# Performance work log

Hardware: AMD Instinct MI355X
Metric: run time of the kernel (lower is better)

## Reference

```python
import jax, jax.numpy as jnp
import numpy as np
import math

B, T, D = 2, 2048, 1024
H = 16
HD = D // H
DFF = 4096
EPS = 1e-5


def setup_inputs() -> dict:
    key = jax.random.key(0)
    ks = jax.random.split(key, 11)
    s = 0.02
    return {
        "x": jax.random.normal(ks[0], (B, T, D), dtype=jnp.float32),
        "scale1": jnp.ones((D,), jnp.float32),
        "scale2": jnp.ones((D,), jnp.float32),
        "Wqkv": jax.random.normal(ks[1], (D, 3 * D), jnp.float32) * s,
        "bqkv": jnp.zeros((3 * D,), jnp.float32),
        "Wo": jax.random.normal(ks[2], (D, D), jnp.float32) * s,
        "bo": jnp.zeros((D,), jnp.float32),
        "W1": jax.random.normal(ks[3], (D, DFF), jnp.float32) * s,
        "b1": jnp.zeros((DFF,), jnp.float32),
        "W2": jax.random.normal(ks[4], (DFF, D), jnp.float32) * s,
        "b2": jnp.zeros((D,), jnp.float32),
    }


def rmsnorm(x, scale):
    # Faithful to source: norm = ||x||/sqrt(d); out = scale * x / (norm + eps)
    d = x.shape[-1]
    norm = jnp.linalg.norm(x, axis=-1, keepdims=True) * (1.0 / math.sqrt(d))
    return scale * x / (norm + EPS)


def attention(x, Wqkv, bqkv, Wo, bo):
    b, t, c = x.shape
    qkv = x @ Wqkv + bqkv                       # [B,T,3D]
    qkv = qkv.reshape(b, t, 3, H, HD)
    q, k, v = qkv[:, :, 0], qkv[:, :, 1], qkv[:, :, 2]   # [B,T,H,HD]
    scores = jnp.einsum("bqhd,bkhd->bhqk", q, k) / math.sqrt(HD)
    w = jax.nn.softmax(scores, axis=-1)
    out = jnp.einsum("bhqk,bkhd->bqhd", w, v).reshape(b, t, c)
    return out @ Wo + bo


def reference(x, scale1, scale2, Wqkv, bqkv, Wo, bo, W1, b1, W2, b2):
    x = x + attention(rmsnorm(x, scale1), Wqkv, bqkv, Wo, bo)
    h = rmsnorm(x, scale2)
    ff = (jax.nn.gelu(h @ W1 + b1, approximate=False)) @ W2 + b2
    return x + ff
```

## Files before the change

kernel.cpp:

```cpp
#include <hip/hip_runtime.h>
#include <hip/hip_bf16.h>
#include <math.h>

typedef unsigned short u16;
typedef __bf16 bf16x8 __attribute__((ext_vector_type(8)));
typedef float f32x4 __attribute__((ext_vector_type(4)));
typedef unsigned int u32x2 __attribute__((ext_vector_type(2)));

#define B_   2
#define T_   2048
#define D_   1024
#define H_   16
#define HD_  64
#define DFF_ 4096
#define M_TOK (B_*T_)

__device__ __forceinline__ u16 f2bf(float f){
  unsigned u = __float_as_uint(f);
  u += 0x7fff + ((u>>16)&1);
  return (u16)(u>>16);
}

__device__ __forceinline__ void gl2lds16(const void* g, void* l){
  __builtin_amdgcn_global_load_lds((const __attribute__((address_space(1))) void*)g,
                                   (__attribute__((address_space(3))) void*)l, 16, 0, 0);
}

__device__ __forceinline__ unsigned lds_u32(const void* p){
  return (unsigned)(uintptr_t)(const __attribute__((address_space(3))) void*)p;
}

__device__ __forceinline__ u32x2 tr_read(unsigned addr){
  u32x2 d;
  asm volatile("ds_read_b64_tr_b16 %0, %1" : "=v"(d) : "v"(addr));
  return d;
}
__device__ __forceinline__ u32x2 tr_read512(unsigned addr){
  u32x2 d;
  asm volatile("ds_read_b64_tr_b16 %0, %1 offset:512" : "=v"(d) : "v"(addr));
  return d;
}
__device__ __forceinline__ bf16x8 pack8(u32x2 a, u32x2 b){
  union { u32x2 u[2]; bf16x8 v; } x; x.u[0]=a; x.u[1]=b; return x.v;
}
__device__ __forceinline__ unsigned cvt_pk_bf16(float a, float b){
  unsigned r;
  asm("v_cvt_pk_bf16_f32 %0, %1, %2" : "=v"(r) : "v"(a), "v"(b));
  return r;
}

__device__ __forceinline__ void block_barrier(){
  asm volatile("" ::: "memory");
  __builtin_amdgcn_s_barrier();
  __builtin_amdgcn_sched_barrier(0);
  asm volatile("" ::: "memory");
}

__device__ __forceinline__ int xcd_chunk(int orig, int nwg){
  int q = nwg >> 3, r = nwg & 7;
  int x = orig & 7, s = orig >> 3;
  return (x < r ? x*(q+1) : r*(q+1) + (x-r)*q) + s;
}

__global__ __launch_bounds__(256) void k_transpose_bf16(const float* __restrict__ in,
                                                        u16* __restrict__ out, int K, int N){
  __shared__ float t[32][33];
  int bx = blockIdx.x*32, by = blockIdx.y*32;
  int tx = threadIdx.x, ty = threadIdx.y;
  #pragma unroll
  for(int i=ty;i<32;i+=8) t[i][tx] = in[(size_t)(by+i)*N + bx + tx];
  __syncthreads();
  #pragma unroll
  for(int i=ty;i<32;i+=8) out[(size_t)(bx+i)*K + by + tx] = f2bf(t[tx][i]);
}

__global__ __launch_bounds__(256) void k_rmsnorm_bf16(const float* __restrict__ x,
                                                      const float* __restrict__ scale,
                                                      u16* __restrict__ out){
  int row = blockIdx.x;
  int tid = threadIdx.x;
  int lane = tid&63, wave = tid>>6;
  const float4* xr = (const float4*)(x + (size_t)row*D_);
  float4 v = xr[tid];
  float ss = v.x*v.x + v.y*v.y + v.z*v.z + v.w*v.w;
  #pragma unroll
  for(int o=1;o<64;o<<=1) ss += __shfl_xor(ss, o);
  __shared__ float red[4];
  if(lane==0) red[wave]=ss;
  __syncthreads();
  float tot = red[0]+red[1]+red[2]+red[3];
  float inv = 1.0f/(sqrtf(tot*(1.0f/D_)) + 1e-5f);
  const float4* sr = (const float4*)scale;
  float4 s4 = sr[tid];
  u16* o4 = out + (size_t)row*D_ + tid*4;
  o4[0]=f2bf(v.x*s4.x*inv); o4[1]=f2bf(v.y*s4.y*inv);
  o4[2]=f2bf(v.z*s4.z*inv); o4[3]=f2bf(v.w*s4.w*inv);
}

template<int EPI>
__global__ __launch_bounds__(512,2) void k_gemm256(const u16* __restrict__ A, const u16* __restrict__ Bt,
                                                   const float* __restrict__ bias,
                                                   void* __restrict__ Cout, int M, int N, int K, int nbx){
  __shared__ u16 LDS[4][16384];
  const int tid = threadIdx.x;
  const int lane = tid&63, wave = tid>>6;
  const int lo = lane&15, hi = lane>>4;
  const int wm = wave>>2, wn = wave&3;
  const int l = xcd_chunk(blockIdx.x, gridDim.x);
  const int row0 = (l % nbx)*256, col0 = (l / nbx)*256;
  f32x4 acc[8][4];
  #pragma unroll
  for(int m=0;m<8;m++)
    #pragma unroll
    for(int n=0;n<4;n++) acc[m][n] = (f32x4){0.f,0.f,0.f,0.f};
  const u16* Ag = A + (size_t)row0*K;
  const u16* Bg = Bt + (size_t)col0*K;
  const int NT = K>>5;

  const int cc0 = tid, cc1 = tid+512;
  const size_t s0 = (size_t)(cc0>>2)*K + (size_t)((((cc0&3)^((cc0>>3)&3)))<<3);
  const size_t s1 = (size_t)(cc1>>2)*K + (size_t)((((cc1&3)^((cc1>>3)&3)))<<3);

  #define STAGE_A(t) { const u16* Ab = Ag + (size_t)(t)*32; char* d = (char*)LDS[(t)&3]; \
    gl2lds16(Ab + s0, d + cc0*16); gl2lds16(Ab + s1, d + cc1*16); }
  #define STAGE_B(t) { const u16* Bb = Bg + (size_t)(t)*32; char* d = (char*)LDS[(t)&3] + 16384; \
    gl2lds16(Bb + s0, d + cc0*16); gl2lds16(Bb + s1, d + cc1*16); }

  STAGE_A(0); STAGE_B(0); STAGE_A(1); STAGE_B(1); STAGE_A(2); STAGE_B(2);

  const unsigned slot = (unsigned)((hi ^ ((lo>>1)&3))<<4);
  for(int t=0;t<NT;t++){
    if(t<NT-2)       { asm volatile("s_waitcnt vmcnt(8)" ::: "memory"); }
    else if(t==NT-2) { asm volatile("s_waitcnt vmcnt(4)" ::: "memory"); }
    else             { asm volatile("s_waitcnt vmcnt(0)" ::: "memory"); }
    block_barrier();
    const char* bufp = (const char*)LDS[t&3];
    const char* ap = bufp + (wm*128 + lo)*64 + slot;
    const char* bp = bufp + 16384 + (wn*64 + lo)*64 + slot;

    if(t+3<NT) STAGE_A(t+3);
    __builtin_amdgcn_sched_barrier(0);
    bf16x8 a0[4], b[4];
    #pragma unroll
    for(int m=0;m<4;m++) a0[m] = *(const bf16x8*)(ap + m*1024);
    #pragma unroll
    for(int n=0;n<4;n++) b[n]  = *(const bf16x8*)(bp + n*1024);
    __builtin_amdgcn_s_setprio(1);
    #pragma unroll
    for(int m=0;m<4;m++)
      #pragma unroll
      for(int n=0;n<4;n++)
        acc[m][n] = __builtin_amdgcn_mfma_f32_16x16x32_bf16(a0[m], b[n], acc[m][n], 0,0,0);
    __builtin_amdgcn_s_setprio(0);

    if(t+3<NT) STAGE_B(t+3);
    __builtin_amdgcn_sched_barrier(0);
    bf16x8 a1[4];
    #pragma unroll
    for(int m=0;m<4;m++) a1[m] = *(const bf16x8*)(ap + 4096 + m*1024);
    __builtin_amdgcn_s_setprio(1);
    #pragma unroll
    for(int m=0;m<4;m++)
      #pragma unroll
      for(int n=0;n<4;n++)
        acc[m+4][n] = __builtin_amdgcn_mfma_f32_16x16x32_bf16(a1[m], b[n], acc[m+4][n], 0,0,0);
    __builtin_amdgcn_s_setprio(0);
  }
  #undef STAGE_A
  #undef STAGE_B

  #pragma unroll
  for(int m=0;m<8;m++){
    #pragma unroll
    for(int n=0;n<4;n++){
      #pragma unroll
      for(int r=0;r<4;r++){
        int row = row0 + wm*128 + m*16 + hi*4 + r;
        int col = col0 + wn*64 + n*16 + lo;
        float v = acc[m][n][r] + bias[col];
        if constexpr(EPI==2){
          v = 0.5f*v*(1.0f + erff(v*0.70710678118f));
        }
        ((u16*)Cout)[(size_t)row*N + col] = f2bf(v);
      }
    }
  }
}

template<int EPI>
__global__ __launch_bounds__(256) void k_gemm(const u16* __restrict__ A, const u16* __restrict__ Bt,
                                              const float* __restrict__ bias, const float* __restrict__ res,
                                              void* __restrict__ Cout, int M, int N, int K, int nbx){
  __shared__ u16 As[128*32];
  __shared__ u16 Bs[128*32];
  int tid = threadIdx.x;
  int lane = tid&63, wave = tid>>6;
  int lo = lane&15, hi = lane>>4;
  int wr = wave>>1, wc = wave&1;
  const int l = xcd_chunk(blockIdx.x, gridDim.x);
  int row0 = (l % nbx)*128, col0 = (l / nbx)*128;
  f32x4 acc[4][4];
  #pragma unroll
  for(int m=0;m<4;m++)
    #pragma unroll
    for(int n=0;n<4;n++) acc[m][n] = (f32x4){0.f,0.f,0.f,0.f};
  const u16* Ag = A + (size_t)row0*K;
  const u16* Bg = Bt + (size_t)col0*K;
  const unsigned sw = (unsigned)((hi^((lo>>1)&3))*16);
  for(int k0=0;k0<K;k0+=32){
    __syncthreads();
    #pragma unroll
    for(int c=tid;c<512;c+=256){
      gl2lds16(Ag + (size_t)(c>>2)*K + k0 + (size_t)(((c&3)^((c>>3)&3))<<3), (char*)As + c*16);
      gl2lds16(Bg + (size_t)(c>>2)*K + k0 + (size_t)(((c&3)^((c>>3)&3))<<3), (char*)Bs + c*16);
    }
    __syncthreads();
    const char* ab = (const char*)As + (wr*64+lo)*64;
    const char* bb = (const char*)Bs + (wc*64+lo)*64;
    bf16x8 a[4], b[4];
    #pragma unroll
    for(int m=0;m<4;m++) a[m] = *(const bf16x8*)(ab + m*1024 + sw);
    #pragma unroll
    for(int n=0;n<4;n++) b[n] = *(const bf16x8*)(bb + n*1024 + sw);
    #pragma unroll
    for(int m=0;m<4;m++)
      #pragma unroll
      for(int n=0;n<4;n++)
        acc[m][n] = __builtin_amdgcn_mfma_f32_16x16x32_bf16(a[m], b[n], acc[m][n], 0,0,0);
  }
  #pragma unroll
  for(int m=0;m<4;m++){
    #pragma unroll
    for(int n=0;n<4;n++){
      #pragma unroll
      for(int r=0;r<4;r++){
        int row = row0 + wr*64 + m*16 + hi*4 + r;
        int col = col0 + wc*64 + n*16 + lo;
        float v = acc[m][n][r] + bias[col];
        if constexpr(EPI==1){
          ((float*)Cout)[(size_t)row*N + col] = v + res[(size_t)row*N + col];
        } else if constexpr(EPI==2){
          v = 0.5f*v*(1.0f + erff(v*0.70710678118f));
          ((u16*)Cout)[(size_t)row*N + col] = f2bf(v);
        } else {
          ((u16*)Cout)[(size_t)row*N + col] = f2bf(v);
        }
      }
    }
  }
}

__global__ __launch_bounds__(256) void k_gemm_pk(const u16* __restrict__ A, const u16* __restrict__ Bt,
                                                 float* __restrict__ P, int M, int N, int K){
  __shared__ u16 As[128*32];
  __shared__ u16 Bs[128*32];
  int tid = threadIdx.x;
  int lane = tid&63, wave = tid>>6;
  int lo = lane&15, hi = lane>>4;
  int wr = wave>>1, wc = wave&1;
  const int l = xcd_chunk(blockIdx.x, gridDim.x);
  const int nbx = M>>7, nby = N>>7;
  int row0 = (l % nbx)*128;
  int col0 = ((l / nbx) % nby)*128;
  int kc   = l / (nbx*nby);
  int klen = K/2, kbeg = kc*klen;
  f32x4 acc[4][4];
  #pragma unroll
  for(int m=0;m<4;m++)
    #pragma unroll
    for(int n=0;n<4;n++) acc[m][n] = (f32x4){0.f,0.f,0.f,0.f};
  const u16* Ag = A + (size_t)row0*K + kbeg;
  const u16* Bg = Bt + (size_t)col0*K + kbeg;
  const unsigned sw = (unsigned)((hi^((lo>>1)&3))*16);
  for(int k0=0;k0<klen;k0+=32){
    __syncthreads();
    #pragma unroll
    for(int c=tid;c<512;c+=256){
      gl2lds16(Ag + (size_t)(c>>2)*K + k0 + (size_t)(((c&3)^((c>>3)&3))<<3), (char*)As + c*16);
      gl2lds16(Bg + (size_t)(c>>2)*K + k0 + (size_t)(((c&3)^((c>>3)&3))<<3), (char*)Bs + c*16);
    }
    __syncthreads();
    const char* ab = (const char*)As + (wr*64+lo)*64;
    const char* bb = (const char*)Bs + (wc*64+lo)*64;
    bf16x8 a[4], b[4];
    #pragma unroll
    for(int m=0;m<4;m++) a[m] = *(const bf16x8*)(ab + m*1024 + sw);
    #pragma unroll
    for(int n=0;n<4;n++) b[n] = *(const bf16x8*)(bb + n*1024 + sw);
    #pragma unroll
    for(int m=0;m<4;m++)
      #pragma unroll
      for(int n=0;n<4;n++)
        acc[m][n] = __builtin_amdgcn_mfma_f32_16x16x32_bf16(a[m], b[n], acc[m][n], 0,0,0);
  }
  float* Pk = P + (size_t)kc*M*N;
  #pragma unroll
  for(int m=0;m<4;m++)
    #pragma unroll
    for(int n=0;n<4;n++)
      #pragma unroll
      for(int r=0;r<4;r++){
        int row = row0 + wr*64 + m*16 + hi*4 + r;
        int col = col0 + wc*64 + n*16 + lo;
        Pk[(size_t)row*N + col] = acc[m][n][r];
      }
}

__global__ __launch_bounds__(256) void k_ff2_reduce(const float* __restrict__ P,
                                                    const float* __restrict__ bias,
                                                    const float* __restrict__ res,
                                                    float* __restrict__ out){
  const size_t total4 = (size_t)M_TOK*D_/4;
  const float4* p0 = (const float4*)P;
  const float4* p1 = (const float4*)(P + (size_t)M_TOK*D_);
  const float4* rr = (const float4*)res;
  const float4* bb = (const float4*)bias;
  float4* oo = (float4*)out;
  for(size_t i = (size_t)blockIdx.x*256 + threadIdx.x; i < total4; i += (size_t)gridDim.x*256){
    float4 a = p0[i], b = p1[i], r = rr[i], c = bb[i & (D_/4 - 1)];
    float4 o;
    o.x = (a.x+b.x)+(c.x+r.x);
    o.y = (a.y+b.y)+(c.y+r.y);
    o.z = (a.z+b.z)+(c.z+r.z);
    o.w = (a.w+b.w)+(c.w+r.w);
    oo[i] = o;
  }
}

__global__ __launch_bounds__(256,4) void k_attn(const u16* __restrict__ qkv, u16* __restrict__ O){
  __shared__ alignas(16) u16 Ks[2][4096];
  __shared__ alignas(16) u16 Vs[2][4096];
  __shared__ alignas(16) u16 Ps[4][1024];
  const int l = xcd_chunk(blockIdx.x, 1024);
  const int qt = l & 31, bh = l >> 5;
  const int h = bh & 15, b = bh >> 4;
  const int tid = threadIdx.x, lane = tid&63, wave = tid>>6;
  const int lo = lane&15, hi = lane>>4, l7 = lane&7;
  const u16* qkvB = qkv + (size_t)b*T_*3072;
  const int hoff = h*64;
  const float C2 = 0.18033688f;

  const int q0 = qt*64 + wave*16;
  const u16* qp = qkvB + (size_t)(q0+lo)*3072 + hoff + hi*8;
  bf16x8 aq0 = *(const bf16x8*)qp;
  bf16x8 aq1 = *(const bf16x8*)(qp+32);

  size_t sK[2], sV[2];
  {
    int cc[2] = {tid, tid+256};
    #pragma unroll
    for(int i=0;i<2;i++){
      int c = cc[i];
      sK[i] = (size_t)(c>>3)*3072 + 1024 + hoff + (((c&7)^((c>>3)&7))<<3);
      int kv = ((c>>5)<<2) + ((c>>1)&3);
      int d0 = (((c&31)>>3)<<4) | ((c&1)<<3);
      sV[i] = (size_t)kv*3072 + 2048 + hoff + d0;
    }
  }
  const unsigned kb0 = (unsigned)lo*128 + (unsigned)((hi^l7))*16;
  const unsigned kb1 = (unsigned)lo*128 + (unsigned)(((hi|4)^l7))*16;
  const unsigned vtr = (unsigned)hi*1024 + (unsigned)lo*2;
  const unsigned swzQ = (unsigned)(lo&7)<<4;

  f32x4 oac[4];
  #pragma unroll
  for(int n=0;n<4;n++) oac[n] = (f32x4){0.f,0.f,0.f,0.f};
  float mrow = -1e30f;
  float lsum = 0.f;

  {
    char* kd = (char*)Ks[0]; char* vd = (char*)Vs[0];
    gl2lds16(qkvB + sK[0], kd + tid*16);
    gl2lds16(qkvB + sK[1], kd + tid*16 + 4096);
    gl2lds16(qkvB + sV[0], vd + tid*16);
    gl2lds16(qkvB + sV[1], vd + tid*16 + 4096);
  }
  int buf = 0;
  for(int t=0;t<T_/64;t++){
    __syncthreads();
    if(t < T_/64-1){
      size_t koff = (size_t)(t+1)*64*3072;
      char* kd = (char*)Ks[buf^1]; char* vd = (char*)Vs[buf^1];
      gl2lds16(qkvB + koff + sK[0], kd + tid*16);
      gl2lds16(qkvB + koff + sK[1], kd + tid*16 + 4096);
      gl2lds16(qkvB + koff + sV[0], vd + tid*16);
      gl2lds16(qkvB + koff + sV[1], vd + tid*16 + 4096);
    }
    const char* K_ = (const char*)Ks[buf];
    u16* P_ = Ps[wave];

    f32x4 s[4];
    __builtin_amdgcn_s_setprio(1);
    #pragma unroll
    for(int n=0;n<4;n++){
      bf16x8 k0f = *(const bf16x8*)(K_ + n*2048 + kb0);
      bf16x8 k1f = *(const bf16x8*)(K_ + n*2048 + kb1);
      f32x4 z = (f32x4){0.f,0.f,0.f,0.f};
      z = __builtin_amdgcn_mfma_f32_16x16x32_bf16(k0f, aq0, z, 0,0,0);
      z = __builtin_amdgcn_mfma_f32_16x16x32_bf16(k1f, aq1, z, 0,0,0);
      s[n] = z;
    }
    __builtin_amdgcn_s_setprio(0);

    float mx = s[0][0];
    #pragma unroll
    for(int n=0;n<4;n++)
      #pragma unroll
      for(int r=0;r<4;r++) mx = fmaxf(mx, s[n][r]);

    if(!__all(mx <= mrow + 64.0f)){
      float mm = fmaxf(mx, __shfl_xor(mx,16));
      mm = fmaxf(mm, __shfl_xor(mm,32));
      float nm = fmaxf(mrow, mm);
      float alpha = exp2f((mrow - nm)*C2);
      mrow = nm;
      lsum *= alpha;
      float ar[4];
      #pragma unroll
      for(int r=0;r<4;r++) ar[r] = __shfl(alpha, hi*4 + r);
      #pragma unroll
      for(int n=0;n<4;n++)
        #pragma unroll
        for(int r=0;r<4;r++) oac[n][r] *= ar[r];
    }

    const float nmC2 = -mrow*C2;
    #pragma unroll
    for(int n=0;n<4;n++){
      float p0v = exp2f(fmaf(s[n][0], C2, nmC2));
      float p1v = exp2f(fmaf(s[n][1], C2, nmC2));
      float p2v = exp2f(fmaf(s[n][2], C2, nmC2));
      float p3v = exp2f(fmaf(s[n][3], C2, nmC2));
      lsum += (p0v+p1v)+(p2v+p3v);
      u32x2 pw;
      pw[0] = cvt_pk_bf16(p0v, p1v);
      pw[1] = cvt_pk_bf16(p2v, p3v);
      *(u32x2*)((char*)P_ + (unsigned)lo*128 + (((unsigned)(n*32 + hi*8)) ^ swzQ)) = pw;
    }

    const unsigned vsb = lds_u32(Vs[buf]);
    #pragma unroll
    for(int kk=0;kk<2;kk++){
      bf16x8 ap = *(const bf16x8*)((const char*)P_ + (kk==0 ? kb0 : kb1));
      u32x2 t0[4], t1[4];
      #pragma unroll
      for(int n=0;n<4;n++){
        unsigned a = vsb + vtr + (unsigned)kk*4096 + (unsigned)n*128;
        t0[n] = tr_read(a);
        t1[n] = tr_read512(a);
      }
      asm volatile("s_waitcnt lgkmcnt(0)" ::: "memory");
      __builtin_amdgcn_sched_barrier(0);
      __builtin_amdgcn_s_setprio(1);
      #pragma unroll
      for(int n=0;n<4;n++){
        bf16x8 bv = pack8(t0[n], t1[n]);
        oac[n] = __builtin_amdgcn_mfma_f32_16x16x32_bf16(ap, bv, oac[n], 0,0,0);
      }
      __builtin_amdgcn_s_setprio(0);
    }
    buf ^= 1;
  }

  lsum += __shfl_xor(lsum, 16);
  lsum += __shfl_xor(lsum, 32);
  float linv = 1.0f/lsum;
  float lr[4];
  #pragma unroll
  for(int r=0;r<4;r++) lr[r] = __shfl(linv, hi*4 + r);
  size_t obase = ((size_t)b*T_ + q0)*D_ + hoff;
  #pragma unroll
  for(int n=0;n<4;n++)
    #pragma unroll
    for(int r=0;r<4;r++)
      O[obase + (size_t)(hi*4+r)*D_ + n*16 + lo] = f2bf(oac[n][r]*lr[r]);
}

extern "C" void kernel_launch(void* const* d_in, const int* in_sizes, int n_in,
                              void* d_out, int out_size, void* d_ws, size_t ws_size,
                              hipStream_t stream){
  (void)in_sizes; (void)n_in; (void)out_size; (void)ws_size;
  const float* x      = (const float*)d_in[0];
  const float* scale1 = (const float*)d_in[1];
  const float* scale2 = (const float*)d_in[2];
  const float* Wqkv   = (const float*)d_in[3];
  const float* bqkv   = (const float*)d_in[4];
  const float* Wo     = (const float*)d_in[5];
  const float* bo     = (const float*)d_in[6];
  const float* W1     = (const float*)d_in[7];
  const float* b1     = (const float*)d_in[8];
  const float* W2     = (const float*)d_in[9];
  const float* b2     = (const float*)d_in[10];
  float* out = (float*)d_out;

  char* w = (char*)d_ws;
  u16* xn1   = (u16*)w;  w += (size_t)M_TOK*D_*2;
  u16* qkvb  = (u16*)w;  w += (size_t)M_TOK*3*D_*2;
  u16* Obuf  = (u16*)w;  w += (size_t)M_TOK*D_*2;
  float* x2  = (float*)w; w += (size_t)M_TOK*D_*4;
  u16* xn2   = (u16*)w;  w += (size_t)M_TOK*D_*2;
  u16* h1    = (u16*)w;  w += (size_t)M_TOK*DFF_*2;
  u16* Wqkvt = (u16*)w;  w += (size_t)3*D_*D_*2;
  u16* Wot   = (u16*)w;  w += (size_t)D_*D_*2;
  u16* W1t   = (u16*)w;  w += (size_t)D_*DFF_*2;
  u16* W2t   = (u16*)w;  w += (size_t)DFF_*D_*2;
  float* pk  = (float*)d_ws;

  dim3 tb(32,8);
  k_transpose_bf16<<<dim3(3*D_/32, D_/32), tb, 0, stream>>>(Wqkv, Wqkvt, D_, 3*D_);
  k_transpose_bf16<<<dim3(D_/32,   D_/32), tb, 0, stream>>>(Wo,   Wot,   D_, D_);
  k_transpose_bf16<<<dim3(DFF_/32, D_/32), tb, 0, stream>>>(W1,   W1t,   D_, DFF_);
  k_transpose_bf16<<<dim3(D_/32, DFF_/32), tb, 0, stream>>>(W2,   W2t,   DFF_, D_);

  k_rmsnorm_bf16<<<M_TOK, 256, 0, stream>>>(x, scale1, xn1);
  k_gemm256<0><<<192, 512, 0, stream>>>(xn1, Wqkvt, bqkv, qkvb, M_TOK, 3*D_, D_, M_TOK/256);
  k_attn<<<1024, 256, 0, stream>>>(qkvb, Obuf);
  k_gemm<1><<<256, 256, 0, stream>>>(Obuf, Wot, bo, x, x2, M_TOK, D_, D_, M_TOK/128);
  k_rmsnorm_bf16<<<M_TOK, 256, 0, stream>>>(x2, scale2, xn2);
  k_gemm256<2><<<256, 512, 0, stream>>>(xn2, W1t, b1, h1, M_TOK, DFF_, D_, M_TOK/256);
  k_gemm_pk<<<512, 256, 0, stream>>>(h1, W2t, pk, M_TOK, D_, DFF_);
  k_ff2_reduce<<<2048, 256, 0, stream>>>(pk, b2, x2, out);
}
```

Measured before the change: 269.7 us.

## Split-K Wo GEMM with fused reduce+RMSNorm, 4-way FF2 split with bf16 partials

The Wo projection moves from a 128x128 tiled GEMM with a residual epilogue to a 2-way split-K GEMM. Its partial sums feed a new kernel that adds bias and residual and also computes the second RMSNorm, which removes the separate rmsnorm pass. The FF2 GEMM goes from 2-way to 4-way split-K, and all split-K partials are stored as bf16 instead of fp32, halving partial-buffer traffic. The aim is better CU occupancy for the small-N GEMMs and fewer memory passes. The cost is precision loss from rounding partial sums to bf16 before they are reduced.

```diff
diff --git a/kernel.cpp b/kernel.cpp
--- a/kernel.cpp
+++ b/kernel.cpp
@@ -20,6 +20,8 @@
   u += 0x7fff + ((u>>16)&1);
   return (u16)(u>>16);
 }
+__device__ __forceinline__ float bflo(unsigned u){ return __uint_as_float(u<<16); }
+__device__ __forceinline__ float bfhi(unsigned u){ return __uint_as_float(u & 0xffff0000u); }
 
 __device__ __forceinline__ void gl2lds16(const void* g, void* l){
   __builtin_amdgcn_global_load_lds((const __attribute__((address_space(1))) void*)g,
@@ -187,71 +189,8 @@
   }
 }
 
-template<int EPI>
-__global__ __launch_bounds__(256) void k_gemm(const u16* __restrict__ A, const u16* __restrict__ Bt,
-                                              const float* __restrict__ bias, const float* __restrict__ res,
-                                              void* __restrict__ Cout, int M, int N, int K, int nbx){
-  __shared__ u16 As[128*32];
-  __shared__ u16 Bs[128*32];
-  int tid = threadIdx.x;
-  int lane = tid&63, wave = tid>>6;
-  int lo = lane&15, hi = lane>>4;
-  int wr = wave>>1, wc = wave&1;
-  const int l = xcd_chunk(blockIdx.x, gridDim.x);
-  int row0 = (l % nbx)*128, col0 = (l / nbx)*128;
-  f32x4 acc[4][4];
-  #pragma unroll
-  for(int m=0;m<4;m++)
-    #pragma unroll
-    for(int n=0;n<4;n++) acc[m][n] = (f32x4){0.f,0.f,0.f,0.f};
-  const u16* Ag = A + (size_t)row0*K;
-  const u16* Bg = Bt + (size_t)col0*K;
-  const unsigned sw = (unsigned)((hi^((lo>>1)&3))*16);
-  for(int k0=0;k0<K;k0+=32){
-    __syncthreads();
-    #pragma unroll
-    for(int c=tid;c<512;c+=256){
-      gl2lds16(Ag + (size_t)(c>>2)*K + k0 + (size_t)(((c&3)^((c>>3)&3))<<3), (char*)As + c*16);
-      gl2lds16(Bg + (size_t)(c>>2)*K + k0 + (size_t)(((c&3)^((c>>3)&3))<<3), (char*)Bs + c*16);
-    }
-    __syncthreads();
-    const char* ab = (const char*)As + (wr*64+lo)*64;
-    const char* bb = (const char*)Bs + (wc*64+lo)*64;
-    bf16x8 a[4], b[4];
-    #pragma unroll
-    for(int m=0;m<4;m++) a[m] = *(const bf16x8*)(ab + m*1024 + sw);
-    #pragma unroll
-    for(int n=0;n<4;n++) b[n] = *(const bf16x8*)(bb + n*1024 + sw);
-    #pragma unroll
-    for(int m=0;m<4;m++)
-      #pragma unroll
-      for(int n=0;n<4;n++)
-        acc[m][n] = __builtin_amdgcn_mfma_f32_16x16x32_bf16(a[m], b[n], acc[m][n], 0,0,0);
-  }
-  #pragma unroll
-  for(int m=0;m<4;m++){
-    #pragma unroll
-    for(int n=0;n<4;n++){
-      #pragma unroll
-      for(int r=0;r<4;r++){
-        int row = row0 + wr*64 + m*16 + hi*4 + r;
-        int col = col0 + wc*64 + n*16 + lo;
-        float v = acc[m][n][r] + bias[col];
-        if constexpr(EPI==1){
-          ((float*)Cout)[(size_t)row*N + col] = v + res[(size_t)row*N + col];
-        } else if constexpr(EPI==2){
-          v = 0.5f*v*(1.0f + erff(v*0.70710678118f));
-          ((u16*)Cout)[(size_t)row*N + col] = f2bf(v);
-        } else {
-          ((u16*)Cout)[(size_t)row*N + col] = f2bf(v);
-        }
-      }
-    }
-  }
-}
-
 __global__ __launch_bounds__(256) void k_gemm_pk(const u16* __restrict__ A, const u16* __restrict__ Bt,
-                                                 float* __restrict__ P, int M, int N, int K){
+                                                 u16* __restrict__ P, int M, int N, int K, int splitk){
   __shared__ u16 As[128*32];
   __shared__ u16 Bs[128*32];
   int tid = threadIdx.x;
@@ -263,7 +202,7 @@
   int row0 = (l % nbx)*128;
   int col0 = ((l / nbx) % nby)*128;
   int kc   = l / (nbx*nby);
-  int klen = K/2, kbeg = kc*klen;
+  int klen = K/splitk, kbeg = kc*klen;
   f32x4 acc[4][4];
   #pragma unroll
   for(int m=0;m<4;m++)
@@ -293,7 +232,7 @@
       for(int n=0;n<4;n++)
         acc[m][n] = __builtin_amdgcn_mfma_f32_16x16x32_bf16(a[m], b[n], acc[m][n], 0,0,0);
   }
-  float* Pk = P + (size_t)kc*M*N;
+  u16* Pk = P + (size_t)kc*M*N;
   #pragma unroll
   for(int m=0;m<4;m++)
     #pragma unroll
@@ -302,29 +241,79 @@
       for(int r=0;r<4;r++){
         int row = row0 + wr*64 + m*16 + hi*4 + r;
         int col = col0 + wc*64 + n*16 + lo;
-        Pk[(size_t)row*N + col] = acc[m][n][r];
+        Pk[(size_t)row*N + col] = f2bf(acc[m][n][r]);
       }
 }
 
-__global__ __launch_bounds__(256) void k_ff2_reduce(const float* __restrict__ P,
-                                                    const float* __restrict__ bias,
-                                                    const float* __restrict__ res,
-                                                    float* __restrict__ out){
-  const size_t total4 = (size_t)M_TOK*D_/4;
-  const float4* p0 = (const float4*)P;
-  const float4* p1 = (const float4*)(P + (size_t)M_TOK*D_);
-  const float4* rr = (const float4*)res;
-  const float4* bb = (const float4*)bias;
-  float4* oo = (float4*)out;
-  for(size_t i = (size_t)blockIdx.x*256 + threadIdx.x; i < total4; i += (size_t)gridDim.x*256){
-    float4 a = p0[i], b = p1[i], r = rr[i], c = bb[i & (D_/4 - 1)];
-    float4 o;
-    o.x = (a.x+b.x)+(c.x+r.x);
-    o.y = (a.y+b.y)+(c.y+r.y);
-    o.z = (a.z+b.z)+(c.z+r.z);
-    o.w = (a.w+b.w)+(c.w+r.w);
-    oo[i] = o;
-  }
+__global__ __launch_bounds__(256) void k_ff2_reduce4(const u16* __restrict__ P,
+                                                     const float* __restrict__ bias,
+                                                     const float* __restrict__ res,
+                                                     float* __restrict__ out){
+  const size_t stride8 = (size_t)M_TOK*D_/8;
+  size_t idx = (size_t)blockIdx.x*256 + threadIdx.x;
+  const uint4* p = (const uint4*)P;
+  uint4 q0 = p[idx], q1 = p[idx+stride8], q2 = p[idx+2*stride8], q3 = p[idx+3*stride8];
+  size_t base = idx*8;
+  const float4* rr = (const float4*)(res + base);
+  const float4* bb = (const float4*)(bias + (base & (D_-1)));
+  float4 r0 = rr[0], r1 = rr[1];
+  float4 b0 = bb[0], b1 = bb[1];
+  float4 o0, o1;
+  unsigned w;
+  w=q0.x; o0.x  = bflo(w); o0.y  = bfhi(w);
+  w=q0.y; o0.z  = bflo(w); o0.w  = bfhi(w);
+  w=q0.z; o1.x  = bflo(w); o1.y  = bfhi(w);
+  w=q0.w; o1.z  = bflo(w); o1.w  = bfhi(w);
+  w=q1.x; o0.x += bflo(w); o0.y += bfhi(w);
+  w=q1.y; o0.z += bflo(w); o0.w += bfhi(w);
+  w=q1.z; o1.x += bflo(w); o1.y += bfhi(w);
+  w=q1.w; o1.z += bflo(w); o1.w += bfhi(w);
+  w=q2.x; o0.x += bflo(w); o0.y += bfhi(w);
+  w=q2.y; o0.z += bflo(w); o0.w += bfhi(w);
+  w=q2.z; o1.x += bflo(w); o1.y += bfhi(w);
+  w=q2.w; o1.z += bflo(w); o1.w += bfhi(w);
+  w=q3.x; o0.x += bflo(w); o0.y += bfhi(w);
+  w=q3.y; o0.z += bflo(w); o0.w += bfhi(w);
+  w=q3.z; o1.x += bflo(w); o1.y += bfhi(w);
+  w=q3.w; o1.z += bflo(w); o1.w += bfhi(w);
+  o0.x += b0.x + r0.x; o0.y += b0.y + r0.y; o0.z += b0.z + r0.z; o0.w += b0.w + r0.w;
+  o1.x += b1.x + r1.x; o1.y += b1.y + r1.y; o1.z += b1.z + r1.z; o1.w += b1.w + r1.w;
+  float4* oo = (float4*)(out + base);
+  oo[0] = o0; oo[1] = o1;
+}
+
+__global__ __launch_bounds__(256) void k_wo_reduce_rms(const u16* __restrict__ P,
+                                                       const float* __restrict__ bo,
+                                                       const float* __restrict__ x,
+                                                       const float* __restrict__ scale2,
+                                                       float* __restrict__ x2,
+                                                       u16* __restrict__ xn2){
+  int row = blockIdx.x;
+  int tid = threadIdx.x;
+  int lane = tid&63, wave = tid>>6;
+  const uint2* p0 = (const uint2*)(P + (size_t)row*D_);
+  const uint2* p1 = (const uint2*)(P + (size_t)M_TOK*D_ + (size_t)row*D_);
+  uint2 a = p0[tid], b = p1[tid];
+  float4 r = ((const float4*)(x + (size_t)row*D_))[tid];
+  float4 bi = ((const float4*)bo)[tid];
+  float4 v;
+  v.x = bflo(a.x) + bflo(b.x) + bi.x + r.x;
+  v.y = bfhi(a.x) + bfhi(b.x) + bi.y + r.y;
+  v.z = bflo(a.y) + bflo(b.y) + bi.z + r.z;
+  v.w = bfhi(a.y) + bfhi(b.y) + bi.w + r.w;
+  ((float4*)(x2 + (size_t)row*D_))[tid] = v;
+  float ss = v.x*v.x + v.y*v.y + v.z*v.z + v.w*v.w;
+  #pragma unroll
+  for(int o=1;o<64;o<<=1) ss += __shfl_xor(ss, o);
+  __shared__ float red[4];
+  if(lane==0) red[wave]=ss;
+  __syncthreads();
+  float tot = red[0]+red[1]+red[2]+red[3];
+  float inv = 1.0f/(sqrtf(tot*(1.0f/D_)) + 1e-5f);
+  float4 s4 = ((const float4*)scale2)[tid];
+  u16* o4 = xn2 + (size_t)row*D_ + tid*4;
+  o4[0]=f2bf(v.x*s4.x*inv); o4[1]=f2bf(v.y*s4.y*inv);
+  o4[2]=f2bf(v.z*s4.z*inv); o4[3]=f2bf(v.w*s4.w*inv);
 }
 
 __global__ __launch_bounds__(256,4) void k_attn(const u16* __restrict__ qkv, u16* __restrict__ O){
@@ -504,7 +493,8 @@
   u16* Wot   = (u16*)w;  w += (size_t)D_*D_*2;
   u16* W1t   = (u16*)w;  w += (size_t)D_*DFF_*2;
   u16* W2t   = (u16*)w;  w += (size_t)DFF_*D_*2;
-  float* pk  = (float*)d_ws;
+  u16* wop = (u16*)d_ws;
+  u16* pkb = (u16*)d_ws;
 
   dim3 tb(32,8);
   k_transpose_bf16<<<dim3(3*D_/32, D_/32), tb, 0, stream>>>(Wqkv, Wqkvt, D_, 3*D_);
@@ -515,9 +505,9 @@
   k_rmsnorm_bf16<<<M_TOK, 256, 0, stream>>>(x, scale1, xn1);
   k_gemm256<0><<<192, 512, 0, stream>>>(xn1, Wqkvt, bqkv, qkvb, M_TOK, 3*D_, D_, M_TOK/256);
   k_attn<<<1024, 256, 0, stream>>>(qkvb, Obuf);
-  k_gemm<1><<<256, 256, 0, stream>>>(Obuf, Wot, bo, x, x2, M_TOK, D_, D_, M_TOK/128);
-  k_rmsnorm_bf16<<<M_TOK, 256, 0, stream>>>(x2, scale2, xn2);
+  k_gemm_pk<<<512, 256, 0, stream>>>(Obuf, Wot, wop, M_TOK, D_, D_, 2);
+  k_wo_reduce_rms<<<M_TOK, 256, 0, stream>>>(wop, bo, x, scale2, x2, xn2);
   k_gemm256<2><<<256, 512, 0, stream>>>(xn2, W1t, b1, h1, M_TOK, DFF_, D_, M_TOK/256);
-  k_gemm_pk<<<512, 256, 0, stream>>>(h1, W2t, pk, M_TOK, D_, DFF_);
-  k_ff2_reduce<<<2048, 256, 0, stream>>>(pk, b2, x2, out);
-}
+  k_gemm_pk<<<1024, 256, 0, stream>>>(h1, W2t, pkb, M_TOK, D_, DFF_, 4);
+  k_ff2_reduce4<<<2048, 256, 0, stream>>>(pkb, b2, x2, out);
+}
```

Result: no change. 270.3 us (+0.2%).
